# Kernel tuning notes

Hardware: AMD Instinct MI355X
Metric: run time of the kernel (lower is better)

Reference implementation:

```python
import jax, jax.numpy as jnp
import numpy as np

T, N, G = 4, 100000, 128
R, B, K = 4, 4096, 32
I = 128


def setup_inputs() -> dict:
    key = jax.random.key(0)
    k1, k2, k3, k4 = jax.random.split(key, 4)
    embeddings = jax.random.normal(k1, (T, N, G), dtype=jnp.float32)
    neighbor_idx = jax.random.randint(k2, (T, R, B, K), 0, N, dtype=jnp.int32)
    neighbor_mask = jax.random.randint(k3, (T, R, B, K), 0, 2).astype(jnp.bool_)
    # xavier_uniform per relation weight [G, I]
    limit = float(np.sqrt(6.0 / (G + I)))
    weights = jax.random.uniform(k4, (R, G, I), dtype=jnp.float32, minval=-limit, maxval=limit)
    return {
        "embeddings": embeddings,
        "weights": weights,
        "neighbor_idx": neighbor_idx,
        "neighbor_mask": neighbor_mask,
        "train_year": T,
    }


def reference(embeddings, weights, neighbor_idx, neighbor_mask, train_year):
    # embeddings: [T, N, G]; neighbor_idx/mask: [T, R, B, K]; weights: [R, G, I]
    m = neighbor_mask.astype(embeddings.dtype)               # [T,R,B,K]
    year = jnp.arange(embeddings.shape[0])[:, None, None, None]
    gathered = embeddings[year, neighbor_idx]                 # [T,R,B,K,G]
    summed = jnp.einsum('trbkg,trbk->trbg', gathered, m)      # masked neighbor sum
    cnt = jnp.maximum(m.sum(-1), 1.0)                         # empty list -> divide by 1 (zeros row)
    mean = summed / cnt[..., None]                            # [T,R,B,G]
    out = jnp.einsum('trbg,rgi->tbi', mean, weights)          # per-relation matmul, sum over R
    return out.reshape(-1, train_year, weights.shape[-1])     # raw flat reshape, as in original
```

## Files before the change

kernel.cpp:

```cpp
#include <hip/hip_runtime.h>

#define T_ 4
#define N_ 100000
#define G_ 128
#define R_ 4
#define B_ 4096
#define K_ 32
#define I_ 128
#define BB 8

__global__ __launch_bounds__(256) void static_influence_kernel(
    const float* __restrict__ E,
    const float* __restrict__ W,
    const int*   __restrict__ idx,
    const int*   __restrict__ msk,
    float*       __restrict__ out)
{
    const int tid = threadIdx.x;
    const int blk = blockIdx.x;
    const int t   = blk / (B_ / BB);
    const int b0  = (blk % (B_ / BB)) * BB;

    __shared__ float mean_s[BB][G_];
    __shared__ int   idxm_s[BB * K_];

    const int wave = tid >> 6;
    const int lane = tid & 63;
    const int half = lane >> 5;
    const int gl   = lane & 31;
    const int bbg  = 2 * wave + half;

    const int iset = tid >> 7;
    const int i    = tid & 127;

    float acc0 = 0.f, acc1 = 0.f, acc2 = 0.f, acc3 = 0.f;

    const float* __restrict__ Et = E + (size_t)t * N_ * G_;

    for (int r = 0; r < R_; ++r) {
        {
            const int base = ((t * R_ + r) * B_ + b0) * K_;
            const int v = idx[base + tid];
            const int m = msk[base + tid];
            idxm_s[tid] = m ? (v | 0x80000000) : v;
        }
        __syncthreads();

        float4 s4 = make_float4(0.f, 0.f, 0.f, 0.f);
        float  cnt = 0.f;
#pragma unroll 8
        for (int k = 0; k < K_; ++k) {
            const int   v  = idxm_s[bbg * K_ + k];
            const int   id = v & 0x7FFFFFFF;
            const float fm = (v < 0) ? 1.0f : 0.0f;
            const float4 e4 = *reinterpret_cast<const float4*>(Et + (size_t)id * G_ + gl * 4);
            s4.x += fm * e4.x;  s4.y += fm * e4.y;
            s4.z += fm * e4.z;  s4.w += fm * e4.w;
            cnt  += fm;
        }
        const float inv = 1.0f / fmaxf(cnt, 1.0f);
        *reinterpret_cast<float4*>(&mean_s[bbg][gl * 4]) =
            make_float4(s4.x * inv, s4.y * inv, s4.z * inv, s4.w * inv);
        __syncthreads();

        const float* __restrict__ Wr = W + r * G_ * I_;
        const int bbm = iset * 4;
#pragma unroll 2
        for (int g = 0; g < G_; g += 4) {
            const float w0 = Wr[(g + 0) * I_ + i];
            const float w1 = Wr[(g + 1) * I_ + i];
            const float w2 = Wr[(g + 2) * I_ + i];
            const float w3 = Wr[(g + 3) * I_ + i];
            const float4 m0 = *reinterpret_cast<const float4*>(&mean_s[bbm + 0][g]);
            const float4 m1 = *reinterpret_cast<const float4*>(&mean_s[bbm + 1][g]);
            const float4 m2 = *reinterpret_cast<const float4*>(&mean_s[bbm + 2][g]);
            const float4 m3 = *reinterpret_cast<const float4*>(&mean_s[bbm + 3][g]);
            acc0 += m0.x * w0 + m0.y * w1 + m0.z * w2 + m0.w * w3;
            acc1 += m1.x * w0 + m1.y * w1 + m1.z * w2 + m1.w * w3;
            acc2 += m2.x * w0 + m2.y * w1 + m2.z * w2 + m2.w * w3;
            acc3 += m3.x * w0 + m3.y * w1 + m3.z * w2 + m3.w * w3;
        }
        __syncthreads();
    }

    const size_t ob = ((size_t)t * B_ + b0 + iset * 4) * I_ + i;
    out[ob + 0 * I_] = acc0;
    out[ob + 1 * I_] = acc1;
    out[ob + 2 * I_] = acc2;
    out[ob + 3 * I_] = acc3;
}

extern "C" void kernel_launch(void* const* d_in, const int* in_sizes, int n_in,
                              void* d_out, int out_size, void* d_ws, size_t ws_size,
                              hipStream_t stream) {
    const float* E   = (const float*)d_in[0];
    const float* W   = (const float*)d_in[1];
    const int*   idx = (const int*)d_in[2];
    const int*   msk = (const int*)d_in[3];
    float* out = (float*)d_out;

    dim3 grid(T_ * (B_ / BB));
    dim3 block(256);
    hipLaunchKernelGGL(static_influence_kernel, grid, block, 0, stream,
                       E, W, idx, msk, out);
}
```

Baseline: 392.6 us.

## Compact masked neighbor lists with ballot and loop over years per block

Uses a wave ballot and popcount to compact the active neighbor indices of each row into shared memory, so that only unmasked embedding rows are gathered rather than loading every neighbor and multiplying by zero. This should roughly halve gather traffic for random masks. The grid also drops from T*512 to 512 blocks, with each block looping over the four years, which lowers occupancy and parallelism. The inner gather loop now has a variable trip count, which can cause imbalance between rows.

```diff
diff --git a/kernel.cpp b/kernel.cpp
--- a/kernel.cpp
+++ b/kernel.cpp
@@ -17,12 +17,11 @@
     float*       __restrict__ out)
 {
     const int tid = threadIdx.x;
-    const int blk = blockIdx.x;
-    const int t   = blk / (B_ / BB);
-    const int b0  = (blk % (B_ / BB)) * BB;
+    const int b0  = blockIdx.x * BB;
 
     __shared__ float mean_s[BB][G_];
-    __shared__ int   idxm_s[BB * K_];
+    __shared__ int   idxc_s[BB * K_];
+    __shared__ int   cnt_s[BB];
 
     const int wave = tid >> 6;
     const int lane = tid & 63;
@@ -33,61 +32,65 @@
     const int iset = tid >> 7;
     const int i    = tid & 127;
 
-    float acc0 = 0.f, acc1 = 0.f, acc2 = 0.f, acc3 = 0.f;
+    for (int t = 0; t < T_; ++t) {
+        const float* __restrict__ Et = E + (size_t)t * N_ * G_;
 
-    const float* __restrict__ Et = E + (size_t)t * N_ * G_;
+        float acc0 = 0.f, acc1 = 0.f, acc2 = 0.f, acc3 = 0.f;
 
-    for (int r = 0; r < R_; ++r) {
-        {
-            const int base = ((t * R_ + r) * B_ + b0) * K_;
-            const int v = idx[base + tid];
-            const int m = msk[base + tid];
-            idxm_s[tid] = m ? (v | 0x80000000) : v;
+        for (int r = 0; r < R_; ++r) {
+            {
+                const int base = ((t * R_ + r) * B_ + b0) * K_;
+                const int  v   = idx[base + tid];
+                const bool act = (msk[base + tid] != 0);
+                const unsigned long long bal = __ballot(act);
+                int rank = __popcll(bal & ((1ULL << lane) - 1));
+                if (half) rank -= __popcll(bal & 0xFFFFFFFFULL);
+                const int row = tid >> 5;
+                if (act) idxc_s[row * K_ + rank] = v;
+                if ((lane & 31) == 0)
+                    cnt_s[row] = __popcll((bal >> (half * 32)) & 0xFFFFFFFFULL);
+            }
+            __syncthreads();
+
+            const int myc = cnt_s[bbg];
+            float4 s4 = make_float4(0.f, 0.f, 0.f, 0.f);
+#pragma unroll 4
+            for (int k = 0; k < myc; ++k) {
+                const int id = idxc_s[bbg * K_ + k];
+                const float4 e4 = *reinterpret_cast<const float4*>(Et + (size_t)id * G_ + gl * 4);
+                s4.x += e4.x;  s4.y += e4.y;  s4.z += e4.z;  s4.w += e4.w;
+            }
+            const float inv = 1.0f / fmaxf((float)myc, 1.0f);
+            *reinterpret_cast<float4*>(&mean_s[bbg][gl * 4]) =
+                make_float4(s4.x * inv, s4.y * inv, s4.z * inv, s4.w * inv);
+            __syncthreads();
+
+            const float* __restrict__ Wr = W + r * G_ * I_;
+            const int bbm = iset * 4;
+#pragma unroll 2
+            for (int g = 0; g < G_; g += 4) {
+                const float w0 = Wr[(g + 0) * I_ + i];
+                const float w1 = Wr[(g + 1) * I_ + i];
+                const float w2 = Wr[(g + 2) * I_ + i];
+                const float w3 = Wr[(g + 3) * I_ + i];
+                const float4 m0 = *reinterpret_cast<const float4*>(&mean_s[bbm + 0][g]);
+                const float4 m1 = *reinterpret_cast<const float4*>(&mean_s[bbm + 1][g]);
+                const float4 m2 = *reinterpret_cast<const float4*>(&mean_s[bbm + 2][g]);
+                const float4 m3 = *reinterpret_cast<const float4*>(&mean_s[bbm + 3][g]);
+                acc0 += m0.x * w0 + m0.y * w1 + m0.z * w2 + m0.w * w3;
+                acc1 += m1.x * w0 + m1.y * w1 + m1.z * w2 + m1.w * w3;
+                acc2 += m2.x * w0 + m2.y * w1 + m2.z * w2 + m2.w * w3;
+                acc3 += m3.x * w0 + m3.y * w1 + m3.z * w2 + m3.w * w3;
+            }
+            __syncthreads();
         }
-        __syncthreads();
 
-        float4 s4 = make_float4(0.f, 0.f, 0.f, 0.f);
-        float  cnt = 0.f;
-#pragma unroll 8
-        for (int k = 0; k < K_; ++k) {
-            const int   v  = idxm_s[bbg * K_ + k];
-            const int   id = v & 0x7FFFFFFF;
-            const float fm = (v < 0) ? 1.0f : 0.0f;
-            const float4 e4 = *reinterpret_cast<const float4*>(Et + (size_t)id * G_ + gl * 4);
-            s4.x += fm * e4.x;  s4.y += fm * e4.y;
-            s4.z += fm * e4.z;  s4.w += fm * e4.w;
-            cnt  += fm;
-        }
-        const float inv = 1.0f / fmaxf(cnt, 1.0f);
-        *reinterpret_cast<float4*>(&mean_s[bbg][gl * 4]) =
-            make_float4(s4.x * inv, s4.y * inv, s4.z * inv, s4.w * inv);
-        __syncthreads();
-
-        const float* __restrict__ Wr = W + r * G_ * I_;
-        const int bbm = iset * 4;
-#pragma unroll 2
-        for (int g = 0; g < G_; g += 4) {
-            const float w0 = Wr[(g + 0) * I_ + i];
-            const float w1 = Wr[(g + 1) * I_ + i];
-            const float w2 = Wr[(g + 2) * I_ + i];
-            const float w3 = Wr[(g + 3) * I_ + i];
-            const float4 m0 = *reinterpret_cast<const float4*>(&mean_s[bbm + 0][g]);
-            const float4 m1 = *reinterpret_cast<const float4*>(&mean_s[bbm + 1][g]);
-            const float4 m2 = *reinterpret_cast<const float4*>(&mean_s[bbm + 2][g]);
-            const float4 m3 = *reinterpret_cast<const float4*>(&mean_s[bbm + 3][g]);
-            acc0 += m0.x * w0 + m0.y * w1 + m0.z * w2 + m0.w * w3;
-            acc1 += m1.x * w0 + m1.y * w1 + m1.z * w2 + m1.w * w3;
-            acc2 += m2.x * w0 + m2.y * w1 + m2.z * w2 + m2.w * w3;
-            acc3 += m3.x * w0 + m3.y * w1 + m3.z * w2 + m3.w * w3;
-        }
-        __syncthreads();
+        const size_t ob = ((size_t)t * B_ + b0 + iset * 4) * I_ + i;
+        out[ob + 0 * I_] = acc0;
+        out[ob + 1 * I_] = acc1;
+        out[ob + 2 * I_] = acc2;
+        out[ob + 3 * I_] = acc3;
     }
-
-    const size_t ob = ((size_t)t * B_ + b0 + iset * 4) * I_ + i;
-    out[ob + 0 * I_] = acc0;
-    out[ob + 1 * I_] = acc1;
-    out[ob + 2 * I_] = acc2;
-    out[ob + 3 * I_] = acc3;
 }
 
 extern "C" void kernel_launch(void* const* d_in, const int* in_sizes, int n_in,
@@ -99,7 +102,7 @@
     const int*   msk = (const int*)d_in[3];
     float* out = (float*)d_out;
 
-    dim3 grid(T_ * (B_ / BB));
+    dim3 grid(B_ / BB);
     dim3 block(256);
     hipLaunchKernelGGL(static_influence_kernel, grid, block, 0, stream,
                        E, W, idx, msk, out);
```

Result: slower. 420.7 us (+7.2%).
